# Performance work log

Measured on AMD Instinct MI355X. Metric: run time of the kernel, lower is better.

Reference implementation:

```python
import jax, jax.numpy as jnp
import numpy as np

FEATURE_MAP = 1024
DIM = 1024
SEQ_LEN = 128
BATCH = 128
WINDOW = 5


def setup_inputs() -> dict:
    key = jax.random.key(0)
    k1, k2 = jax.random.split(key)
    x = jax.random.normal(k1, (BATCH, SEQ_LEN, DIM), dtype=jnp.float32)
    # xavier-uniform-ish scale for Ws
    limit = np.sqrt(6.0 / (DIM + FEATURE_MAP)).astype(np.float32)
    Ws = jax.random.uniform(k2, (WINDOW, DIM, FEATURE_MAP), dtype=jnp.float32,
                            minval=-limit, maxval=limit)
    b = jnp.zeros((FEATURE_MAP,), dtype=jnp.float32)
    return {"x": x, "Ws": Ws, "b": b}


def reference(x, Ws, b):
    # x: [B, L, D] batch-first -> work in time-major order like the original.
    # Precompute all 5 projections for every timestep in one big einsum:
    # proj: [L, W, B, F]
    proj = jnp.einsum('bld,wdf->lwbf', x, Ws)
    B = x.shape[0]
    h0 = jnp.zeros((WINDOW, B, FEATURE_MAP), dtype=x.dtype)

    def step(h, p):
        # h, p: [W, B, F]
        # m1 = max(p0, h1); m_k = max(h_{k-1} + p_k, h_k) for k>=2 (old h used)
        cand = jnp.concatenate([p[:1], h[:-1] + p[1:]], axis=0)
        new_h = jnp.maximum(cand, h)
        return new_h, None

    h_final, _ = jax.lax.scan(step, h0, proj)
    return jnp.tanh(h_final[WINDOW - 1] + b[None, :])  # [B, F]
```

## Files before the change

kernel.cpp:

```cpp
#include <hip/hip_runtime.h>
#include <hip/hip_bf16.h>

#define WINDOW 5
#define DIM 1024
#define FEAT 1024
#define SEQ 128
#define BATCH 128
#define MTOT (BATCH*SEQ)
#define NTOT (WINDOW*FEAT)
#define KTOT 1024

#define DCHUNK 16

typedef int int4v __attribute__((ext_vector_type(4)));

static __device__ __forceinline__ unsigned short f2bf(float f) {
  union { float f; unsigned int i; } c; c.f = f;
  unsigned int i = c.i;
  unsigned int lsb = (i >> 16) & 1u;
  i += 0x7fffu + lsb;
  return (unsigned short)(i >> 16);
}
static __device__ __forceinline__ float bf2f(unsigned short u) {
  union { unsigned int i; float f; } c; c.i = ((unsigned int)u) << 16; return c.f;
}
static __device__ __forceinline__ signed char q8(float v, float inv) {
  float q = rintf(v * inv);
  q = fminf(fmaxf(q, -127.f), 127.f);
  return (signed char)(int)q;
}

__global__ __launch_bounds__(256) void quant_x(const float* __restrict__ x,
                                               signed char* __restrict__ xq,
                                               float* __restrict__ sx) {
  int row  = blockIdx.x * 4 + (threadIdx.x >> 6);
  int lane = threadIdx.x & 63;
  const float* xr = x + (size_t)row * KTOT;

  float4 v[4];
  float amax = 0.f;
  #pragma unroll
  for (int i = 0; i < 4; i++) {
    v[i] = ((const float4*)xr)[i * 64 + lane];
    amax = fmaxf(amax, fmaxf(fmaxf(fabsf(v[i].x), fabsf(v[i].y)),
                             fmaxf(fabsf(v[i].z), fabsf(v[i].w))));
  }
  #pragma unroll
  for (int m = 1; m < 64; m <<= 1)
    amax = fmaxf(amax, __shfl_xor(amax, m));

  float inv = amax > 0.f ? 127.f / amax : 0.f;
  int* xqr = (int*)(xq + (size_t)row * KTOT);
  #pragma unroll
  for (int i = 0; i < 4; i++) {
    int p = ((int)(unsigned char)q8(v[i].x, inv)) |
            ((int)(unsigned char)q8(v[i].y, inv) << 8) |
            ((int)(unsigned char)q8(v[i].z, inv) << 16) |
            ((int)q8(v[i].w, inv) << 24);
    xqr[i * 64 + lane] = p;
  }
  if (lane == 0) sx[row] = amax / 127.f;
}

__global__ __launch_bounds__(256) void w_colamax_part(const float* __restrict__ Ws,
                                                      float* __restrict__ part) {
  int w  = blockIdx.z;
  int dc = blockIdx.y;
  int f4 = threadIdx.x;
  const float* p = Ws + ((size_t)w * DIM + (size_t)dc * DCHUNK) * FEAT;
  float4 m = {0.f, 0.f, 0.f, 0.f};
  #pragma unroll
  for (int d = 0; d < DCHUNK; d++) {
    float4 v = ((const float4*)(p + (size_t)d * FEAT))[f4];
    m.x = fmaxf(m.x, fabsf(v.x));
    m.y = fmaxf(m.y, fabsf(v.y));
    m.z = fmaxf(m.z, fabsf(v.z));
    m.w = fmaxf(m.w, fabsf(v.w));
  }
  ((float4*)(part + ((size_t)w * (DIM / DCHUNK) + dc) * FEAT))[f4] = m;
}

__global__ __launch_bounds__(256) void w_colamax_reduce(const float* __restrict__ part,
                                                        float* __restrict__ sw) {
  int idx = blockIdx.x * 256 + threadIdx.x;
  int w = idx >> 10, f = idx & 1023;
  const float* p = part + (size_t)w * (DIM / DCHUNK) * FEAT + f;
  float m = 0.f;
  #pragma unroll 8
  for (int c = 0; c < DIM / DCHUNK; c++)
    m = fmaxf(m, p[(size_t)c * FEAT]);
  sw[idx] = m / 127.f;
}

__global__ __launch_bounds__(256) void transq_ws(const float* __restrict__ Ws,
                                                 const float* __restrict__ sw,
                                                 signed char* __restrict__ wq) {
  __shared__ float tile[32][33];
  int w  = blockIdx.z;
  int f0 = blockIdx.x * 32, d0 = blockIdx.y * 32;
  int tx = threadIdx.x, ty = threadIdx.y;
  const float* src = Ws + ((size_t)w * DIM + d0) * FEAT + f0;
  #pragma unroll
  for (int i = 0; i < 4; i++)
    tile[ty + 8*i][tx] = src[(size_t)(ty + 8*i) * FEAT + tx];
  __syncthreads();
  signed char* dst = wq + ((size_t)w * FEAT + f0) * DIM + d0;
  #pragma unroll
  for (int i = 0; i < 4; i++) {
    int f = f0 + ty + 8*i;
    float swv = sw[(w << 10) + f];
    float inv = swv > 0.f ? 1.0f / swv : 0.f;
    dst[(size_t)(ty + 8*i) * DIM + tx] = q8(tile[tx][ty + 8*i], inv);
  }
}

__global__ __launch_bounds__(512, 2) void fused_gemm_scan(
    const signed char* __restrict__ xq,
    const signed char* __restrict__ wq,
    const float* __restrict__ sx,
    const float* __restrict__ swp,
    const float* __restrict__ bias,
    float* __restrict__ out)
{
  __shared__ __align__(16) char smem[81920];
  signed char* As = (signed char*)smem;
  signed char* Bs = (signed char*)(smem + 16384);

  const int tid  = threadIdx.x;
  const int wid  = tid >> 6;
  const int lane = tid & 63;

  int bid = blockIdx.x;
  int wg  = ((bid & 7) << 8) + (bid >> 3);
  const int b  = wg >> 4;
  const int f0 = (wg & 15) << 6;

  const signed char* aG = xq + (size_t)b * SEQ * KTOT;

  const int wm = wid >> 2, wn = wid & 3;
  const int rowin = lane >> 3;
  const int swb16 = ((lane & 7) ^ rowin) << 4;

  int4v acc[4][5];
  #pragma unroll
  for (int i = 0; i < 4; i++)
    #pragma unroll
    for (int j = 0; j < 5; j++)
      acc[i][j] = (int4v){0, 0, 0, 0};

  for (int kt = 0; kt < 8; kt++) {
    const int k0 = kt << 7;
    #pragma unroll
    for (int c = 0; c < 7; c++) {
      int seg = wid * 7 + c;
      if (seg < 16) {
        int row = (seg << 3) + rowin;
        __builtin_amdgcn_global_load_lds(
            (const __attribute__((address_space(1))) void*)(aG + (size_t)row * KTOT + k0 + swb16),
            (__attribute__((address_space(3))) void*)(As + (seg << 10)), 16, 0, 0);
      } else {
        int sb = seg - 16;
        int r  = (sb << 3) + rowin;
        const signed char* src = wq
            + ((size_t)(((r >> 6) << 10) + f0 + (r & 63))) * KTOT + k0 + swb16;
        __builtin_amdgcn_global_load_lds(
            (const __attribute__((address_space(1))) void*)src,
            (__attribute__((address_space(3))) void*)(Bs + (sb << 10)), 16, 0, 0);
      }
    }
    __syncthreads();

    #pragma unroll
    for (int kk = 0; kk < 2; kk++) {
      int4v a[4], bf[5];
      #pragma unroll
      for (int i = 0; i < 4; i++) {
        int row  = wm * 64 + i * 16 + (lane & 15);
        int slot = (lane >> 4) + (kk << 2);
        a[i] = *(const int4v*)(As + row * 128 + ((slot ^ (row & 7)) << 4));
      }
      #pragma unroll
      for (int j = 0; j < 5; j++) {
        int row  = wn * 80 + j * 16 + (lane & 15);
        int slot = (lane >> 4) + (kk << 2);
        bf[j] = *(const int4v*)(Bs + row * 128 + ((slot ^ (row & 7)) << 4));
      }
      #pragma unroll
      for (int i = 0; i < 4; i++)
        #pragma unroll
        for (int j = 0; j < 5; j++)
          acc[i][j] = __builtin_amdgcn_mfma_i32_16x16x64_i8(a[i], bf[j], acc[i][j], 0, 0, 0);
    }
    __syncthreads();
  }

  float sxv[16];
  #pragma unroll
  for (int i = 0; i < 4; i++)
    #pragma unroll
    for (int r = 0; r < 4; r++)
      sxv[i * 4 + r] = sx[b * SEQ + wm * 64 + i * 16 + ((lane >> 4) << 2) + r];
  float swv[5];
  #pragma unroll
  for (int j = 0; j < 5; j++) {
    int c = wn * 80 + j * 16 + (lane & 15);
    swv[j] = swp[((c >> 6) << 10) + f0 + (c & 63)];
  }

  #pragma unroll
  for (int i = 0; i < 4; i++) {
    #pragma unroll
    for (int j = 0; j < 5; j++) {
      #pragma unroll
      for (int r = 0; r < 4; r++) {
        int l = wm * 64 + i * 16 + ((lane >> 4) << 2) + r;
        int c = wn * 80 + j * 16 + (lane & 15);
        float v = (float)acc[i][j][r] * sxv[i * 4 + r] * swv[j];
        int byte = ((l * 320 + c) << 1) ^ (((l >> 2) & 3) << 5);
        *(unsigned short*)(smem + byte) = f2bf(v);
      }
    }
  }
  __syncthreads();

  if (tid < 64) {
    const int fl = tid;
    float h0 = 0.f, h1 = 0.f, h2 = 0.f, h3 = 0.f, h4 = 0.f;
    for (int l = 0; l < SEQ; l++) {
      const int swz  = ((l >> 2) & 3) << 5;
      const int base = l * 640;
      float p[5];
      #pragma unroll
      for (int w = 0; w < 5; w++) {
        int byte = (base + (((w << 6) + fl) << 1)) ^ swz;
        p[w] = bf2f(*(const unsigned short*)(smem + byte));
      }
      h4 = fmaxf(h3 + p[4], h4);
      h3 = fmaxf(h2 + p[3], h3);
      h2 = fmaxf(h1 + p[2], h2);
      h1 = fmaxf(h0 + p[1], h1);
      h0 = fmaxf(p[0], h0);
    }
    out[b * FEAT + f0 + fl] = tanhf(h4 + bias[f0 + fl]);
  }
}

extern "C" void kernel_launch(void* const* d_in, const int* in_sizes, int n_in,
                              void* d_out, int out_size, void* d_ws, size_t ws_size,
                              hipStream_t stream) {
  const float* x  = (const float*)d_in[0];
  const float* Ws = (const float*)d_in[1];
  const float* b  = (const float*)d_in[2];
  float* out = (float*)d_out;

  char* ws = (char*)d_ws;
  const size_t XQ_BYTES = (size_t)MTOT * KTOT;
  const size_t WQ_BYTES = (size_t)WINDOW * FEAT * DIM;
  const size_t SX_BYTES = (size_t)MTOT * 4;
  const size_t SW_BYTES = (size_t)WINDOW * FEAT * 4;
  signed char* xq = (signed char*)ws;
  signed char* wq = (signed char*)(ws + XQ_BYTES);
  float* sx   = (float*)(ws + XQ_BYTES + WQ_BYTES);
  float* sw   = (float*)(ws + XQ_BYTES + WQ_BYTES + SX_BYTES);
  float* part = (float*)(ws + XQ_BYTES + WQ_BYTES + SX_BYTES + SW_BYTES);

  hipLaunchKernelGGL(quant_x, dim3(MTOT / 4), dim3(256), 0, stream, x, xq, sx);
  hipLaunchKernelGGL(w_colamax_part, dim3(1, DIM / DCHUNK, WINDOW), dim3(256), 0, stream,
                     Ws, part);
  hipLaunchKernelGGL(w_colamax_reduce, dim3(NTOT / 256), dim3(256), 0, stream, part, sw);
  hipLaunchKernelGGL(transq_ws, dim3(FEAT / 32, DIM / 32, WINDOW), dim3(32, 8), 0, stream,
                     Ws, sw, wq);
  hipLaunchKernelGGL(fused_gemm_scan, dim3(BATCH * 16), dim3(512), 0, stream,
                     xq, wq, sx, sw, b, out);
}
```

Measured before the change: 174.7 us.

## Double-buffer LDS K-tiles and parallelize scan across all warps

The GEMM main loop now prefetches the next K-tile into a second LDS buffer using global_load_lds, waiting with a partial vmcnt before a raw s_barrier, so loads overlap the MFMA work. MFMA sections are wrapped in s_setprio. The epilogue scan, previously run by a single 64-thread wave, is spread over all 512 threads: each window slot is handled by a lane and the previous slot is fetched by shuffle. LDS use grows to 112KB per block, which likely limits occupancy to one block per CU despite the launch bounds of two.

```diff
diff --git a/kernel.cpp b/kernel.cpp
--- a/kernel.cpp
+++ b/kernel.cpp
@@ -11,6 +11,7 @@
 #define KTOT 1024
 
 #define DCHUNK 16
+#define BUFB 57344
 
 typedef int int4v __attribute__((ext_vector_type(4)));
 
@@ -122,9 +123,7 @@
     const float* __restrict__ bias,
     float* __restrict__ out)
 {
-  __shared__ __align__(16) char smem[81920];
-  signed char* As = (signed char*)smem;
-  signed char* Bs = (signed char*)(smem + 16384);
+  __shared__ __align__(16) char smem[2 * BUFB];
 
   const int tid  = threadIdx.x;
   const int wid  = tid >> 6;
@@ -141,6 +140,31 @@
   const int rowin = lane >> 3;
   const int swb16 = ((lane & 7) ^ rowin) << 4;
 
+  #define STAGE(kt_, base_)                                                        \
+    do {                                                                           \
+      signed char* As_ = (signed char*)(base_);                                    \
+      signed char* Bs_ = (signed char*)(base_) + 16384;                            \
+      const int k0_ = (kt_) << 7;                                                  \
+      _Pragma("unroll")                                                            \
+      for (int c_ = 0; c_ < 7; c_++) {                                             \
+        int seg_ = wid * 7 + c_;                                                   \
+        if (seg_ < 16) {                                                           \
+          int row_ = (seg_ << 3) + rowin;                                          \
+          __builtin_amdgcn_global_load_lds(                                        \
+              (const __attribute__((address_space(1))) void*)(aG + (size_t)row_ * KTOT + k0_ + swb16), \
+              (__attribute__((address_space(3))) void*)(As_ + (seg_ << 10)), 16, 0, 0); \
+        } else {                                                                   \
+          int sb_ = seg_ - 16;                                                     \
+          int r_  = (sb_ << 3) + rowin;                                            \
+          const signed char* src_ = wq                                             \
+              + ((size_t)(((r_ >> 6) << 10) + f0 + (r_ & 63))) * KTOT + k0_ + swb16; \
+          __builtin_amdgcn_global_load_lds(                                        \
+              (const __attribute__((address_space(1))) void*)src_,                 \
+              (__attribute__((address_space(3))) void*)(Bs_ + (sb_ << 10)), 16, 0, 0); \
+        }                                                                          \
+      }                                                                            \
+    } while (0)
+
   int4v acc[4][5];
   #pragma unroll
   for (int i = 0; i < 4; i++)
@@ -148,28 +172,23 @@
     for (int j = 0; j < 5; j++)
       acc[i][j] = (int4v){0, 0, 0, 0};
 
+  STAGE(0, smem);
+
   for (int kt = 0; kt < 8; kt++) {
-    const int k0 = kt << 7;
-    #pragma unroll
-    for (int c = 0; c < 7; c++) {
-      int seg = wid * 7 + c;
-      if (seg < 16) {
-        int row = (seg << 3) + rowin;
-        __builtin_amdgcn_global_load_lds(
-            (const __attribute__((address_space(1))) void*)(aG + (size_t)row * KTOT + k0 + swb16),
-            (__attribute__((address_space(3))) void*)(As + (seg << 10)), 16, 0, 0);
-      } else {
-        int sb = seg - 16;
-        int r  = (sb << 3) + rowin;
-        const signed char* src = wq
-            + ((size_t)(((r >> 6) << 10) + f0 + (r & 63))) * KTOT + k0 + swb16;
-        __builtin_amdgcn_global_load_lds(
-            (const __attribute__((address_space(1))) void*)src,
-            (__attribute__((address_space(3))) void*)(Bs + (sb << 10)), 16, 0, 0);
-      }
-    }
-    __syncthreads();
-
+    char* cur = smem + (size_t)(kt & 1) * BUFB;
+    if (kt < 7) {
+      STAGE(kt + 1, smem + (size_t)((kt + 1) & 1) * BUFB);
+      __builtin_amdgcn_sched_barrier(0);
+      asm volatile("s_waitcnt vmcnt(7)" ::: "memory");
+    } else {
+      __builtin_amdgcn_sched_barrier(0);
+      asm volatile("s_waitcnt vmcnt(0)" ::: "memory");
+    }
+    __builtin_amdgcn_s_barrier();
+    __builtin_amdgcn_sched_barrier(0);
+
+    const signed char* As = (const signed char*)cur;
+    const signed char* Bs = (const signed char*)cur + 16384;
     #pragma unroll
     for (int kk = 0; kk < 2; kk++) {
       int4v a[4], bf[5];
@@ -185,14 +204,18 @@
         int slot = (lane >> 4) + (kk << 2);
         bf[j] = *(const int4v*)(Bs + row * 128 + ((slot ^ (row & 7)) << 4));
       }
+      __builtin_amdgcn_s_setprio(1);
       #pragma unroll
       for (int i = 0; i < 4; i++)
         #pragma unroll
         for (int j = 0; j < 5; j++)
           acc[i][j] = __builtin_amdgcn_mfma_i32_16x16x64_i8(a[i], bf[j], acc[i][j], 0, 0, 0);
-    }
-    __syncthreads();
-  }
+      __builtin_amdgcn_s_setprio(0);
+    }
+    __builtin_amdgcn_s_barrier();
+  }
+
+  __syncthreads();
 
   float sxv[16];
   #pragma unroll
@@ -223,26 +246,23 @@
   }
   __syncthreads();
 
-  if (tid < 64) {
-    const int fl = tid;
-    float h0 = 0.f, h1 = 0.f, h2 = 0.f, h3 = 0.f, h4 = 0.f;
+  {
+    const int f = tid >> 3;
+    const int k = tid & 7;
+    float h = 0.f;
     for (int l = 0; l < SEQ; l++) {
-      const int swz  = ((l >> 2) & 3) << 5;
-      const int base = l * 640;
-      float p[5];
-      #pragma unroll
-      for (int w = 0; w < 5; w++) {
-        int byte = (base + (((w << 6) + fl) << 1)) ^ swz;
-        p[w] = bf2f(*(const unsigned short*)(smem + byte));
-      }
-      h4 = fmaxf(h3 + p[4], h4);
-      h3 = fmaxf(h2 + p[3], h3);
-      h2 = fmaxf(h1 + p[2], h2);
-      h1 = fmaxf(h0 + p[1], h1);
-      h0 = fmaxf(p[0], h0);
-    }
-    out[b * FEAT + f0 + fl] = tanhf(h4 + bias[f0 + fl]);
-  }
+      float p = 0.f;
+      if (k < 5) {
+        int byte = (l * 640 + (((k << 6) + f) << 1)) ^ (((l >> 2) & 3) << 5);
+        p = bf2f(*(const unsigned short*)(smem + byte));
+      }
+      float hprev = __shfl(h, (lane - 1) & 63);
+      h = (k == 0) ? fmaxf(p, h) : fmaxf(hprev + p, h);
+    }
+    if (k == 4)
+      out[b * FEAT + f0 + f] = tanhf(h + bias[f0 + f]);
+  }
+  #undef STAGE
 }
 
 extern "C" void kernel_launch(void* const* d_in, const int* in_sizes, int n_in,
```

New measurement: 222.4 us. 27.3% more time.
